# Kernel optimization log

Hardware: AMD Instinct MI355X
Metric: run time of the kernel (lower is better)

The kernel has to match this reference:

```python
import jax, jax.numpy as jnp
import numpy as np

D_MODEL = 2048
NUM_HEADS = 16
D_K = D_MODEL // NUM_HEADS


def setup_inputs() -> dict:
    key = jax.random.key(0)
    ks = jax.random.split(key, 12)
    B, S, D = 2, 2048, D_MODEL
    s = 1.0 / np.sqrt(D)
    return {
        "q": jax.random.normal(ks[0], (B, S, D), jnp.float32),
        "k": jax.random.normal(ks[1], (B, S, D), jnp.float32),
        "v": jax.random.normal(ks[2], (B, S, D), jnp.float32),
        "Wq": jax.random.normal(ks[3], (D, D), jnp.float32) * s,
        "bq": jax.random.normal(ks[4], (D,), jnp.float32) * 0.01,
        "Wk": jax.random.normal(ks[5], (D, D), jnp.float32) * s,
        "bk": jax.random.normal(ks[6], (D,), jnp.float32) * 0.01,
        "Wv": jax.random.normal(ks[7], (D, D), jnp.float32) * s,
        "bv": jax.random.normal(ks[8], (D,), jnp.float32) * 0.01,
        "Wo": jax.random.normal(ks[9], (D, D), jnp.float32) * s,
        "bo": jax.random.normal(ks[10], (D,), jnp.float32) * 0.01,
    }


def reference(q, k, v, Wq, bq, Wk, bk, Wv, bv, Wo, bo):
    B, S, D = q.shape
    H, dk = NUM_HEADS, D_K

    def proj(x, W, b):
        # Linear then split heads -> [B, H, S, dk]
        y = jnp.einsum('bsd,df->bsf', x, W) + b
        return y.reshape(B, -1, H, dk).transpose(0, 2, 1, 3)

    Q = proj(q, Wq, bq)
    K = proj(k, Wk, bk)
    V = proj(v, Wv, bv)

    scores = jnp.einsum('bhqd,bhkd->bhqk', Q, K) / jnp.sqrt(jnp.float32(dk))
    attn = jax.nn.softmax(scores, axis=-1)  # dropout is identity (eval)
    out = jnp.einsum('bhqk,bhkd->bhqd', attn, V)
    out = out.transpose(0, 2, 1, 3).reshape(B, -1, D)
    return jnp.einsum('bsd,df->bsf', out, Wo) + bo
```

## Files before the change

kernel.cpp:

```cpp
#include <hip/hip_runtime.h>
#include <hip/hip_bf16.h>
#include <stdint.h>

typedef float  f32x4  __attribute__((ext_vector_type(4)));
typedef float  f32x16 __attribute__((ext_vector_type(16)));
typedef short  s16x8  __attribute__((ext_vector_type(8)));

#define D_MODEL 2048
#define NHEADS  16
#define DK      128
#define BATCH   2
#define SEQ     2048
#define MROWS   (BATCH*SEQ)

__device__ __forceinline__ unsigned short f2bf(float f) {
  union { float f; unsigned int u; } v; v.f = f;
  unsigned int r = v.u + 0x7FFFu + ((v.u >> 16) & 1u);
  return (unsigned short)(r >> 16);
}

__device__ __forceinline__ unsigned int packbf_c(float lo, float hi) {
  __hip_bfloat16 l = __float2bfloat16(lo);
  __hip_bfloat16 h = __float2bfloat16(hi);
  unsigned short lu, hu;
  __builtin_memcpy(&lu, &l, 2);
  __builtin_memcpy(&hu, &h, 2);
  return (unsigned int)lu | ((unsigned int)hu << 16);
}

__device__ __forceinline__ void async16(const void* g, void* l) {
  __builtin_amdgcn_global_load_lds(
      (const __attribute__((address_space(1))) unsigned int*)g,
      (__attribute__((address_space(3))) unsigned int*)l,
      16, 0, 0);
}

__global__ __launch_bounds__(256) void f2b3_kernel(const float* __restrict__ q,
                                                   const float* __restrict__ k,
                                                   const float* __restrict__ v,
                                                   unsigned short* __restrict__ qb,
                                                   unsigned short* __restrict__ kb,
                                                   unsigned short* __restrict__ vb) {
  const float* s; unsigned short* d;
  switch (blockIdx.y) {
    case 0:  s = q; d = qb; break;
    case 1:  s = k; d = kb; break;
    default: s = v; d = vb; break;
  }
  int i = blockIdx.x * 256 + threadIdx.x;
  const float4* s4 = (const float4*)s;
  float4 a = s4[2*i];
  float4 b = s4[2*i+1];
  s16x8 o;
  o[0] = (short)f2bf(a.x); o[1] = (short)f2bf(a.y);
  o[2] = (short)f2bf(a.z); o[3] = (short)f2bf(a.w);
  o[4] = (short)f2bf(b.x); o[5] = (short)f2bf(b.y);
  o[6] = (short)f2bf(b.z); o[7] = (short)f2bf(b.w);
  *(s16x8*)(d + 8*(size_t)i) = o;
}

__global__ __launch_bounds__(256) void wtrans_kernel(const float* __restrict__ Wq,
                                                     const float* __restrict__ Wk,
                                                     const float* __restrict__ Wv,
                                                     const float* __restrict__ Wo,
                                                     unsigned short* __restrict__ WqT,
                                                     unsigned short* __restrict__ WkT,
                                                     unsigned short* __restrict__ WvT,
                                                     unsigned short* __restrict__ WoT) {
  const float* W; unsigned short* Wt;
  switch (blockIdx.z) {
    case 0:  W = Wq; Wt = WqT; break;
    case 1:  W = Wk; Wt = WkT; break;
    case 2:  W = Wv; Wt = WvT; break;
    default: W = Wo; Wt = WoT; break;
  }
  __shared__ float tl[32][33];
  int x = threadIdx.x, y = threadIdx.y;
  int n0 = blockIdx.x * 32, k0 = blockIdx.y * 32;
  #pragma unroll
  for (int j = 0; j < 32; j += 8)
    tl[y + j][x] = W[(size_t)(k0 + y + j) * D_MODEL + n0 + x];
  __syncthreads();
  #pragma unroll
  for (int j = 0; j < 32; j += 8)
    Wt[(size_t)(n0 + y + j) * D_MODEL + k0 + x] = f2bf(tl[x][y + j]);
}

__device__ __forceinline__ void gemm3b_core(const unsigned short* __restrict__ A,
                                            const unsigned short* __restrict__ Bt,
                                            const float* __restrict__ bias,
                                            void* __restrict__ Cout,
                                            int N, int K, int mode, float scale,
                                            int m0, int n0, char* lds) {
  const int t  = threadIdx.x;
  const int l  = t & 63, w = t >> 6;
  const int wm = w >> 1, wn = w & 1;
  const int lr = l & 15, lg = l >> 4;

  auto STAGE = [&](int slot, int kt) {
    char* Ad = lds + slot*49152;
    char* Bd = lds + slot*49152 + 32768;
    #pragma unroll
    for (int i = 0; i < 4; ++i) {
      int c = t + 512*i;
      int row = c >> 3, crs = (c & 7) ^ (row & 7);
      async16(A + (size_t)(m0 + row)*K + kt*64 + crs*8, Ad + c*16);
    }
    #pragma unroll
    for (int i = 0; i < 2; ++i) {
      int c = t + 512*i;
      int row = c >> 3, crs = (c & 7) ^ (row & 7);
      async16(Bt + (size_t)(n0 + row)*K + kt*64 + crs*8, Bd + c*16);
    }
  };

  const int NT = K >> 6;
  STAGE(0, 0);
  STAGE(1, 1);
  asm volatile("s_waitcnt vmcnt(6)" ::: "memory");
  __builtin_amdgcn_s_barrier();

  f32x4 acc[4][4] = {};

  for (int kt = 0; kt < NT; ++kt) {
    if (kt + 2 < NT) STAGE((kt + 2) % 3, kt + 2);
    const char* Ac = lds + (kt % 3)*49152;
    const char* Bc = lds + (kt % 3)*49152 + 32768;

    #pragma unroll
    for (int ks = 0; ks < 2; ++ks) {
      const int cb = ks*64 + lg*16;
      s16x8 af[4], bf[4];
      #pragma unroll
      for (int mf = 0; mf < 4; ++mf) {
        int row = wm*64 + mf*16 + lr;
        af[mf] = *(const s16x8*)(Ac + row*128 + (cb ^ ((row & 7) << 4)));
      }
      #pragma unroll
      for (int nf = 0; nf < 4; ++nf) {
        int row = wn*64 + nf*16 + lr;
        bf[nf] = *(const s16x8*)(Bc + row*128 + (cb ^ ((row & 7) << 4)));
      }
      __builtin_amdgcn_s_setprio(1);
      #pragma unroll
      for (int mf = 0; mf < 4; ++mf)
        #pragma unroll
        for (int nf = 0; nf < 4; ++nf)
          acc[mf][nf] = __builtin_amdgcn_mfma_f32_16x16x32_bf16(af[mf], bf[nf], acc[mf][nf], 0, 0, 0);
      __builtin_amdgcn_s_setprio(0);
    }

    if (kt + 1 < NT) {
      if (kt + 2 < NT) asm volatile("s_waitcnt vmcnt(6)" ::: "memory");
      else             asm volatile("s_waitcnt vmcnt(0)" ::: "memory");
      __builtin_amdgcn_s_barrier();
    }
  }

  if (mode == 0) {
    float* C = (float*)Cout;
    #pragma unroll
    for (int nf = 0; nf < 4; ++nf) {
      int col = n0 + wn*64 + nf*16 + lr;
      float bv = bias[col];
      #pragma unroll
      for (int mf = 0; mf < 4; ++mf) {
        int rowb = m0 + wm*64 + mf*16 + lg*4;
        #pragma unroll
        for (int r = 0; r < 4; ++r)
          C[(size_t)(rowb + r)*N + col] = (acc[mf][nf][r] + bv) * scale;
      }
    }
  } else {
    unsigned short* C = (unsigned short*)Cout;
    #pragma unroll
    for (int nf = 0; nf < 4; ++nf) {
      int col = n0 + wn*64 + nf*16 + lr;
      float bv = bias[col];
      int h = col >> 7, dkk = col & 127;
      #pragma unroll
      for (int mf = 0; mf < 4; ++mf) {
        int rowb = m0 + wm*64 + mf*16 + lg*4;
        #pragma unroll
        for (int r = 0; r < 4; ++r) {
          int row = rowb + r;
          int b = row >> 11, s = row & 2047;
          C[((size_t)((b*NHEADS + h)*SEQ + s))*DK + dkk] = f2bf((acc[mf][nf][r] + bv) * scale);
        }
      }
    }
  }
}

__device__ __forceinline__ void swz_mn(int& m0, int& n0) {
  int lin = blockIdx.y * 16 + blockIdx.x;
  int xcd = lin & 7;
  int pos = lin >> 3;
  n0 = (xcd*2 + (pos & 1)) * 128;
  m0 = (pos >> 1) * 256;
}

__global__ __launch_bounds__(512) void gemm256_qkv(const unsigned short* __restrict__ qb,
                                                   const unsigned short* __restrict__ kb,
                                                   const unsigned short* __restrict__ vb,
                                                   const unsigned short* __restrict__ WT,
                                                   const float* __restrict__ bq,
                                                   const float* __restrict__ bk,
                                                   const float* __restrict__ bv,
                                                   unsigned short* __restrict__ Hout,
                                                   float qscale) {
  __shared__ char lds[147456];
  const int z = blockIdx.z;
  const unsigned short* A = (z == 0) ? qb : (z == 1) ? kb : vb;
  const float* bias       = (z == 0) ? bq : (z == 1) ? bk : bv;
  const float scale       = (z == 0) ? qscale : 1.0f;
  const unsigned short* Bt = WT + (size_t)z * D_MODEL * D_MODEL;
  unsigned short* Cout     = Hout + (size_t)z * MROWS * D_MODEL;
  int m0, n0; swz_mn(m0, n0);
  gemm3b_core(A, Bt, bias, Cout, D_MODEL, D_MODEL, 1, scale, m0, n0, lds);
}

__global__ __launch_bounds__(512) void gemm256_out(const unsigned short* __restrict__ A,
                                                   const unsigned short* __restrict__ Bt,
                                                   const float* __restrict__ bias,
                                                   float* __restrict__ Cout) {
  __shared__ char lds[147456];
  int m0, n0; swz_mn(m0, n0);
  gemm3b_core(A, Bt, bias, Cout, D_MODEL, D_MODEL, 0, 1.0f, m0, n0, lds);
}

__global__ __launch_bounds__(256, 2) void attn_kernel(const unsigned short* __restrict__ Q,
                                                      const unsigned short* __restrict__ K,
                                                      const unsigned short* __restrict__ V,
                                                      unsigned short* __restrict__ O) {
  __shared__ char lds[64*256 + 128*144];
  unsigned short* Kl = (unsigned short*)lds;
  unsigned short* Vt = (unsigned short*)(lds + 64*256);

  const int t  = threadIdx.x;
  const int l  = t & 63, w = t >> 6;
  const int q_ = l & 31, hi = l >> 5;
  const int bh = blockIdx.y;
  const int b  = bh >> 4, h = bh & 15;
  const int q0 = blockIdx.x * 128;

  const unsigned short* Qp = Q + (size_t)bh * SEQ * DK;
  const unsigned short* Kp = K + (size_t)bh * SEQ * DK;
  const unsigned short* Vp = V + (size_t)bh * SEQ * DK;

  const int qrow = q0 + w*32 + q_;
  s16x8 aq[8];
  #pragma unroll
  for (int kk = 0; kk < 8; ++kk)
    aq[kk] = *(const s16x8*)(Qp + (size_t)qrow*DK + kk*16 + hi*8);

  f32x16 accO[4] = {};
  float m = -INFINITY, L = 0.f;

  const int vp_ = t & 31;
  const int vd0 = (t >> 5) * 8;

  const int NT = SEQ/64;
  s16x8 va0, vb0, va1, vb1;

  va0 = *(const s16x8*)(Vp + (size_t)(2*vp_    )*DK + vd0);
  vb0 = *(const s16x8*)(Vp + (size_t)(2*vp_ + 1)*DK + vd0);
  va1 = *(const s16x8*)(Vp + (size_t)(2*vp_    )*DK + vd0 + 64);
  vb1 = *(const s16x8*)(Vp + (size_t)(2*vp_ + 1)*DK + vd0 + 64);
  #pragma unroll
  for (int i = 0; i < 4; ++i) {
    int c   = t + 256*i;
    int row = c >> 4;
    int sb  = ((c & 15) << 4) ^ ((row & 15) << 4);
    async16((const char*)(Kp + (size_t)row*DK) + sb, (char*)Kl + c*16);
  }
  asm volatile("" ::: "memory");

  for (int tt = 0; tt < NT; ++tt) {
    asm volatile("s_waitcnt vmcnt(4)" ::: "memory");
    #pragma unroll
    for (int j = 0; j < 8; ++j) {
      unsigned int pk0 = (unsigned int)(unsigned short)va0[j]
                       | ((unsigned int)(unsigned short)vb0[j] << 16);
      *(unsigned int*)&Vt[(vd0 + j)*72 + 2*vp_] = pk0;
      unsigned int pk1 = (unsigned int)(unsigned short)va1[j]
                       | ((unsigned int)(unsigned short)vb1[j] << 16);
      *(unsigned int*)&Vt[(vd0 + 64 + j)*72 + 2*vp_] = pk1;
    }
    __syncthreads();

    f32x16 S0 = {}, S1 = {};
    #pragma unroll
    for (int t2 = 0; t2 < 2; ++t2) {
      int krow = t2*32 + q_;
      const char* kb = (const char*)Kl + krow*256;
      int swz = (krow & 15) << 4;
      #pragma unroll
      for (int kk = 0; kk < 8; ++kk) {
        s16x8 kf = *(const s16x8*)(kb + ((kk*32 + hi*16) ^ swz));
        if (t2 == 0) S0 = __builtin_amdgcn_mfma_f32_32x32x16_bf16(kf, aq[kk], S0, 0, 0, 0);
        else         S1 = __builtin_amdgcn_mfma_f32_32x32x16_bf16(kf, aq[kk], S1, 0, 0, 0);
      }
    }
    __syncthreads();

    if (tt + 1 < NT) {
      int kvn = (tt + 1) * 64;
      va0 = *(const s16x8*)(Vp + (size_t)(kvn + 2*vp_    )*DK + vd0);
      vb0 = *(const s16x8*)(Vp + (size_t)(kvn + 2*vp_ + 1)*DK + vd0);
      va1 = *(const s16x8*)(Vp + (size_t)(kvn + 2*vp_    )*DK + vd0 + 64);
      vb1 = *(const s16x8*)(Vp + (size_t)(kvn + 2*vp_ + 1)*DK + vd0 + 64);
      #pragma unroll
      for (int i = 0; i < 4; ++i) {
        int c   = t + 256*i;
        int row = c >> 4;
        int sb  = ((c & 15) << 4) ^ ((row & 15) << 4);
        async16((const char*)(Kp + (size_t)(kvn + row)*DK) + sb, (char*)Kl + c*16);
      }
      asm volatile("" ::: "memory");
    }

    f32x16 mx;
    #pragma unroll
    for (int r = 0; r < 16; ++r) mx[r] = fmaxf(S0[r], S1[r]);
    float m8_[8];
    #pragma unroll
    for (int r = 0; r < 8; ++r) m8_[r] = fmaxf(mx[r], mx[r+8]);
    float m4a = fmaxf(m8_[0], m8_[4]), m4b = fmaxf(m8_[1], m8_[5]);
    float m4c = fmaxf(m8_[2], m8_[6]), m4d = fmaxf(m8_[3], m8_[7]);
    float pmax = fmaxf(fmaxf(m4a, m4b), fmaxf(m4c, m4d));
    pmax = fmaxf(pmax, __shfl_xor(pmax, 32, 64));

    if (!__all(pmax <= m + 11.0f)) {
      float mnew = fmaxf(m, pmax);
      float corr = exp2f(m - mnew);
      m = mnew;
      L *= corr;
      #pragma unroll
      for (int sub = 0; sub < 4; ++sub)
        #pragma unroll
        for (int r = 0; r < 16; ++r) accO[sub][r] *= corr;
    }

    float rs0 = 0.f, rs1 = 0.f, rs2 = 0.f, rs3 = 0.f;
    #pragma unroll
    for (int r = 0; r < 4; ++r) {
      float a0 = exp2f(S0[r]    - m); S0[r]    = a0; rs0 += a0;
      float a1 = exp2f(S0[r+4]  - m); S0[r+4]  = a1; rs1 += a1;
      float a2 = exp2f(S0[r+8]  - m); S0[r+8]  = a2; rs2 += a2;
      float a3 = exp2f(S0[r+12] - m); S0[r+12] = a3; rs3 += a3;
      float b0 = exp2f(S1[r]    - m); S1[r]    = b0; rs0 += b0;
      float b1 = exp2f(S1[r+4]  - m); S1[r+4]  = b1; rs1 += b1;
      float b2 = exp2f(S1[r+8]  - m); S1[r+8]  = b2; rs2 += b2;
      float b3 = exp2f(S1[r+12] - m); S1[r+12] = b3; rs3 += b3;
    }
    float rs = (rs0 + rs1) + (rs2 + rs3);
    rs += __shfl_xor(rs, 32, 64);
    L += rs;

    s16x8 PB[4];
    #pragma unroll
    for (int t2 = 0; t2 < 2; ++t2) {
      #pragma unroll
      for (int half = 0; half < 2; ++half) {
        int bse = half*8;
        unsigned int pkA01, pkA23, pkB01, pkB23;
        if (t2 == 0) {
          pkA01 = packbf_c(S0[bse+0], S0[bse+1]);
          pkA23 = packbf_c(S0[bse+2], S0[bse+3]);
          pkB01 = packbf_c(S0[bse+4], S0[bse+5]);
          pkB23 = packbf_c(S0[bse+6], S0[bse+7]);
        } else {
          pkA01 = packbf_c(S1[bse+0], S1[bse+1]);
          pkA23 = packbf_c(S1[bse+2], S1[bse+3]);
          pkB01 = packbf_c(S1[bse+4], S1[bse+5]);
          pkB23 = packbf_c(S1[bse+6], S1[bse+7]);
        }
        unsigned int xA01 = __shfl_xor(pkA01, 32, 64);
        unsigned int xA23 = __shfl_xor(pkA23, 32, 64);
        unsigned int xB01 = __shfl_xor(pkB01, 32, 64);
        unsigned int xB23 = __shfl_xor(pkB23, 32, 64);
        union { unsigned int u[4]; s16x8 v; } f;
        f.u[0] = hi ? xB01 : pkA01;
        f.u[1] = hi ? xB23 : pkA23;
        f.u[2] = hi ? pkB01 : xA01;
        f.u[3] = hi ? pkB23 : xA23;
        PB[t2*2 + half] = f.v;
      }
    }

    #pragma unroll
    for (int sub = 0; sub < 4; ++sub) {
      const char* vb2 = (const char*)Vt + (size_t)(sub*32 + q_)*144 + hi*16;
      #pragma unroll
      for (int kk = 0; kk < 4; ++kk) {
        s16x8 vf = *(const s16x8*)(vb2 + kk*32);
        accO[sub] = __builtin_amdgcn_mfma_f32_32x32x16_bf16(vf, PB[kk], accO[sub], 0, 0, 0);
      }
    }

    __builtin_amdgcn_s_barrier();
  }

  __syncthreads();
  unsigned short* Ob = (unsigned short*)lds + (size_t)w*4096;
  float inv = 1.0f / L;
  #pragma unroll
  for (int sub = 0; sub < 4; ++sub)
    #pragma unroll
    for (int j = 0; j < 8; ++j) {
      unsigned int pw = packbf_c(accO[sub][2*j]*inv, accO[sub][2*j+1]*inv);
      int dv = sub*32 + (j&1)*2 + ((j>>1)*8) + 4*hi;
      *(unsigned int*)((char*)Ob + q_*256 + ((dv*2) ^ ((q_ & 15) << 4))) = pw;
    }
  asm volatile("s_waitcnt lgkmcnt(0)" ::: "memory");
  size_t gbase = ((size_t)(b*SEQ + q0 + w*32 + q_))*D_MODEL + h*DK;
  #pragma unroll
  for (int p = 0; p < 8; ++p) {
    int chunk = hi + 2*p;
    s16x8 ov = *(const s16x8*)((char*)Ob + q_*256 + ((chunk*16) ^ ((q_ & 15) << 4)));
    *(s16x8*)(O + gbase + chunk*8) = ov;
  }
}

extern "C" void kernel_launch(void* const* d_in, const int* in_sizes, int n_in,
                              void* d_out, int out_size, void* d_ws, size_t ws_size,
                              hipStream_t stream) {
  const float* q  = (const float*)d_in[0];
  const float* k  = (const float*)d_in[1];
  const float* v  = (const float*)d_in[2];
  const float* Wq = (const float*)d_in[3];
  const float* bq = (const float*)d_in[4];
  const float* Wk = (const float*)d_in[5];
  const float* bk = (const float*)d_in[6];
  const float* Wv = (const float*)d_in[7];
  const float* bv = (const float*)d_in[8];
  const float* Wo = (const float*)d_in[9];
  const float* bo = (const float*)d_in[10];
  float* out = (float*)d_out;

  char* ws = (char*)d_ws;
  const size_t SZT = (size_t)MROWS * D_MODEL * 2;
  const size_t SZW = (size_t)D_MODEL * D_MODEL * 2;

  unsigned short* qb  = (unsigned short*)(ws);
  unsigned short* kb  = (unsigned short*)(ws + SZT);
  unsigned short* vb  = (unsigned short*)(ws + 2*SZT);
  unsigned short* WqT = (unsigned short*)(ws + 3*SZT);
  unsigned short* WkT = (unsigned short*)(ws + 3*SZT + SZW);
  unsigned short* WvT = (unsigned short*)(ws + 3*SZT + 2*SZW);
  unsigned short* WoT = (unsigned short*)(ws + 3*SZT + 3*SZW);
  unsigned short* Qh  = (unsigned short*)(ws + 3*SZT + 4*SZW);
  unsigned short* Kh  = (unsigned short*)(ws + 4*SZT + 4*SZW);
  unsigned short* Vh  = (unsigned short*)(ws + 5*SZT + 4*SZW);
  unsigned short* Oc  = qb;

  const int n8 = MROWS * D_MODEL / 8;
  f2b3_kernel<<<dim3(n8/256, 3), 256, 0, stream>>>(q, k, v, qb, kb, vb);
  wtrans_kernel<<<dim3(64, 64, 4), dim3(32, 8), 0, stream>>>(Wq, Wk, Wv, Wo, WqT, WkT, WvT, WoT);

  const float qscale = 0.1275174308f;
  gemm256_qkv<<<dim3(16, 16, 3), 512, 0, stream>>>(qb, kb, vb, WqT, bq, bk, bv, Qh, qscale);

  attn_kernel<<<dim3(SEQ/128, BATCH*NHEADS), 256, 0, stream>>>(Qh, Kh, Vh, Oc);

  gemm256_out<<<dim3(16, 16), 512, 0, stream>>>(Oc, WoT, bo, out);
}
```

Measured before the change: 306.7 us.

## Split attention KV range in two and merge partial results in combine kernel

Adds a z-dimension to the attention grid so each block processes half of the key/value sequence. Each block writes unnormalized bf16 partial outputs plus per-row (max, sum) statistics. A new combine kernel merges the two halves with softmax rescaling before the output projection. This doubles the block count to expose more parallelism. In exchange it adds an extra kernel launch, extra global traffic for the partial outputs, and a bf16 rounding of unnormalized accumulators.

Measured after the change: 318.8 us. +3.9%, slower.

```diff
diff --git a/kernel.cpp b/kernel.cpp
--- a/kernel.cpp
+++ b/kernel.cpp
@@ -17,6 +17,11 @@
   union { float f; unsigned int u; } v; v.f = f;
   unsigned int r = v.u + 0x7FFFu + ((v.u >> 16) & 1u);
   return (unsigned short)(r >> 16);
+}
+
+__device__ __forceinline__ float bf2f(unsigned short u) {
+  union { unsigned int u; float f; } v; v.u = (unsigned int)u << 16;
+  return v.f;
 }
 
 __device__ __forceinline__ unsigned int packbf_c(float lo, float hi) {
@@ -232,7 +237,8 @@
 __global__ __launch_bounds__(256, 2) void attn_kernel(const unsigned short* __restrict__ Q,
                                                       const unsigned short* __restrict__ K,
                                                       const unsigned short* __restrict__ V,
-                                                      unsigned short* __restrict__ O) {
+                                                      unsigned short* __restrict__ Up,
+                                                      float2* __restrict__ ML) {
   __shared__ char lds[64*256 + 128*144];
   unsigned short* Kl = (unsigned short*)lds;
   unsigned short* Vt = (unsigned short*)(lds + 64*256);
@@ -243,6 +249,8 @@
   const int bh = blockIdx.y;
   const int b  = bh >> 4, h = bh & 15;
   const int q0 = blockIdx.x * 128;
+  const int z  = blockIdx.z;
+  const int kvs = z * (SEQ/2);
 
   const unsigned short* Qp = Q + (size_t)bh * SEQ * DK;
   const unsigned short* Kp = K + (size_t)bh * SEQ * DK;
@@ -260,23 +268,23 @@
   const int vp_ = t & 31;
   const int vd0 = (t >> 5) * 8;
 
-  const int NT = SEQ/64;
+  const int NT2 = SEQ/128;
   s16x8 va0, vb0, va1, vb1;
 
-  va0 = *(const s16x8*)(Vp + (size_t)(2*vp_    )*DK + vd0);
-  vb0 = *(const s16x8*)(Vp + (size_t)(2*vp_ + 1)*DK + vd0);
-  va1 = *(const s16x8*)(Vp + (size_t)(2*vp_    )*DK + vd0 + 64);
-  vb1 = *(const s16x8*)(Vp + (size_t)(2*vp_ + 1)*DK + vd0 + 64);
+  va0 = *(const s16x8*)(Vp + (size_t)(kvs + 2*vp_    )*DK + vd0);
+  vb0 = *(const s16x8*)(Vp + (size_t)(kvs + 2*vp_ + 1)*DK + vd0);
+  va1 = *(const s16x8*)(Vp + (size_t)(kvs + 2*vp_    )*DK + vd0 + 64);
+  vb1 = *(const s16x8*)(Vp + (size_t)(kvs + 2*vp_ + 1)*DK + vd0 + 64);
   #pragma unroll
   for (int i = 0; i < 4; ++i) {
     int c   = t + 256*i;
     int row = c >> 4;
     int sb  = ((c & 15) << 4) ^ ((row & 15) << 4);
-    async16((const char*)(Kp + (size_t)row*DK) + sb, (char*)Kl + c*16);
+    async16((const char*)(Kp + (size_t)(kvs + row)*DK) + sb, (char*)Kl + c*16);
   }
   asm volatile("" ::: "memory");
 
-  for (int tt = 0; tt < NT; ++tt) {
+  for (int tt = 0; tt < NT2; ++tt) {
     asm volatile("s_waitcnt vmcnt(4)" ::: "memory");
     #pragma unroll
     for (int j = 0; j < 8; ++j) {
@@ -304,8 +312,8 @@
     }
     __syncthreads();
 
-    if (tt + 1 < NT) {
-      int kvn = (tt + 1) * 64;
+    if (tt + 1 < NT2) {
+      int kvn = kvs + (tt + 1) * 64;
       va0 = *(const s16x8*)(Vp + (size_t)(kvn + 2*vp_    )*DK + vd0);
       vb0 = *(const s16x8*)(Vp + (size_t)(kvn + 2*vp_ + 1)*DK + vd0);
       va1 = *(const s16x8*)(Vp + (size_t)(kvn + 2*vp_    )*DK + vd0 + 64);
@@ -404,23 +412,52 @@
 
   __syncthreads();
   unsigned short* Ob = (unsigned short*)lds + (size_t)w*4096;
-  float inv = 1.0f / L;
   #pragma unroll
   for (int sub = 0; sub < 4; ++sub)
     #pragma unroll
     for (int j = 0; j < 8; ++j) {
-      unsigned int pw = packbf_c(accO[sub][2*j]*inv, accO[sub][2*j+1]*inv);
+      unsigned int pw = packbf_c(accO[sub][2*j], accO[sub][2*j+1]);
       int dv = sub*32 + (j&1)*2 + ((j>>1)*8) + 4*hi;
       *(unsigned int*)((char*)Ob + q_*256 + ((dv*2) ^ ((q_ & 15) << 4))) = pw;
     }
+  if (hi == 0)
+    ML[(size_t)z * (BATCH*NHEADS*SEQ) + (size_t)bh*SEQ + q0 + w*32 + q_] = make_float2(m, L);
   asm volatile("s_waitcnt lgkmcnt(0)" ::: "memory");
+  unsigned short* U = Up + (size_t)z * MROWS * D_MODEL;
   size_t gbase = ((size_t)(b*SEQ + q0 + w*32 + q_))*D_MODEL + h*DK;
   #pragma unroll
   for (int p = 0; p < 8; ++p) {
     int chunk = hi + 2*p;
     s16x8 ov = *(const s16x8*)((char*)Ob + q_*256 + ((chunk*16) ^ ((q_ & 15) << 4)));
-    *(s16x8*)(O + gbase + chunk*8) = ov;
-  }
+    *(s16x8*)(U + gbase + chunk*8) = ov;
+  }
+}
+
+__global__ __launch_bounds__(256) void combine_kernel(const unsigned short* __restrict__ Up,
+                                                      const float2* __restrict__ ML,
+                                                      unsigned short* __restrict__ Oc) {
+  int idx = blockIdx.x * 256 + threadIdx.x;
+  int dv8 = idx & 15;
+  int h   = (idx >> 4) & 15;
+  int row = idx >> 8;
+  int b = row >> 11, s = row & 2047;
+  int bh = b*NHEADS + h;
+
+  float2 ml0 = ML[(size_t)bh*SEQ + s];
+  float2 ml1 = ML[(size_t)(BATCH*NHEADS*SEQ) + (size_t)bh*SEQ + s];
+  float mmax = fmaxf(ml0.x, ml1.x);
+  float a0 = exp2f(ml0.x - mmax), a1 = exp2f(ml1.x - mmax);
+  float den = a0*ml0.y + a1*ml1.y;
+  float w0 = a0 / den, w1 = a1 / den;
+
+  size_t off = (size_t)row * D_MODEL + h*DK + dv8*8;
+  s16x8 u0 = *(const s16x8*)(Up + off);
+  s16x8 u1 = *(const s16x8*)(Up + (size_t)MROWS*D_MODEL + off);
+  s16x8 o;
+  #pragma unroll
+  for (int j = 0; j < 8; ++j)
+    o[j] = (short)f2bf(w0*bf2f((unsigned short)u0[j]) + w1*bf2f((unsigned short)u1[j]));
+  *(s16x8*)(Oc + off) = o;
 }
 
 extern "C" void kernel_launch(void* const* d_in, const int* in_sizes, int n_in,
@@ -453,7 +490,9 @@
   unsigned short* Qh  = (unsigned short*)(ws + 3*SZT + 4*SZW);
   unsigned short* Kh  = (unsigned short*)(ws + 4*SZT + 4*SZW);
   unsigned short* Vh  = (unsigned short*)(ws + 5*SZT + 4*SZW);
-  unsigned short* Oc  = qb;
+  unsigned short* Up  = qb;
+  float2*         ML  = (float2*)vb;
+  unsigned short* Oc  = WqT;
 
   const int n8 = MROWS * D_MODEL / 8;
   f2b3_kernel<<<dim3(n8/256, 3), 256, 0, stream>>>(q, k, v, qb, kb, vb);
@@ -462,7 +501,8 @@
   const float qscale = 0.1275174308f;
   gemm256_qkv<<<dim3(16, 16, 3), 512, 0, stream>>>(qb, kb, vb, WqT, bq, bk, bv, Qh, qscale);
 
-  attn_kernel<<<dim3(SEQ/128, BATCH*NHEADS), 256, 0, stream>>>(Qh, Kh, Vh, Oc);
+  attn_kernel<<<dim3(SEQ/128, BATCH*NHEADS, 2), 256, 0, stream>>>(Qh, Kh, Vh, Up, ML);
+  combine_kernel<<<dim3(MROWS * D_MODEL / 8 / 256), 256, 0, stream>>>(Up, ML, Oc);
 
   gemm256_out<<<dim3(16, 16), 512, 0, stream>>>(Oc, WoT, bo, out);
 }
```
